# Performance work log

Hardware: AMD Instinct MI355X
Metric: run time of the kernel (lower is better)

## Reference

```python
import jax, jax.numpy as jnp
import numpy as np

B, S, E, D = 8, 2048, 512, 512  # batch, seq (mesh edges), elem_size, embd_size


def setup_inputs() -> dict:
    key = jax.random.key(0)
    ks = jax.random.split(key, 5)
    scale = 1.0 / np.sqrt(E)
    return {
        "x": jax.random.normal(ks[0], (B, S, E), dtype=jnp.float32),
        "Wq": jax.random.normal(ks[1], (E, D), dtype=jnp.float32) * scale,
        "bq": jax.random.normal(ks[2], (D,), dtype=jnp.float32) * 0.01,
        "Wk": jax.random.normal(ks[3], (E, D), dtype=jnp.float32) * scale,
        "bk": jax.random.normal(ks[4], (D,), dtype=jnp.float32) * 0.01,
    }


def reference(x, Wq, bq, Wk, bk):
    elem_size = x.shape[-1]
    q = jax.nn.relu(x @ Wq + bq)              # [B,S,D]
    k = jax.nn.relu(x @ Wk + bk)              # [B,S,D]
    scores = jnp.einsum("bqd,bkd->bqk", q, k) / (elem_size ** 0.5)  # [B,S,S]
    # nn.Softmax(dim=1): normalize over the QUERY axis (column-wise softmax)
    attn = jax.nn.softmax(scores, axis=1)
    new_values = jnp.einsum("bqk,bke->bqe", attn, x)  # V = raw x (use_V=False)
    return x + new_values                     # residual connection
```

## Files before the change

kernel.cpp:

```cpp
#include <hip/hip_runtime.h>
#include <hip/hip_bf16.h>
#include <math.h>

#define Bb 8
#define Ss 2048
#define Ee 512
#define Dd 512
#define QSPLIT 16

typedef __bf16 bf16x8 __attribute__((ext_vector_type(8)));
typedef __bf16 bf16x4 __attribute__((ext_vector_type(4)));
typedef float f32x4 __attribute__((ext_vector_type(4)));


__device__ __forceinline__ void stage64(ushort* lds, const __bf16* gbase,
                                        int ldg, int wave, int lane) {
#pragma unroll
    for (int t = 0; t < 4; ++t) {
        const int slot = wave * 256 + t * 64 + lane;
        const int row  = slot >> 3;
        const int c    = (slot & 7) ^ (row & 7);
        __builtin_amdgcn_global_load_lds(
            (const __attribute__((address_space(1))) void*)(gbase + (size_t)row * ldg + c * 8),
            (__attribute__((address_space(3))) void*)(lds + (size_t)slot * 8),
            16, 0, 0);
    }
}

__device__ __forceinline__ void stage64h(ushort* lds, const __bf16* gbase,
                                         int ldg, int wave, int lane) {
#pragma unroll
    for (int t = 0; t < 2; ++t) {
        const int slot = wave * 128 + t * 64 + lane;
        const int row  = slot >> 3;
        const int c    = (slot & 7) ^ (row & 7);
        __builtin_amdgcn_global_load_lds(
            (const __attribute__((address_space(1))) void*)(gbase + (size_t)row * ldg + c * 8),
            (__attribute__((address_space(3))) void*)(lds + (size_t)slot * 8),
            16, 0, 0);
    }
}

__device__ __forceinline__ void stage32(ushort* lds, const __bf16* gbase,
                                        int ldg, int wave, int lane) {
#pragma unroll
    for (int t = 0; t < 2; ++t) {
        const int slot = wave * 128 + t * 64 + lane;
        const int row  = slot >> 2;
        const int c    = (slot & 3) ^ ((row >> 1) & 3);
        __builtin_amdgcn_global_load_lds(
            (const __attribute__((address_space(1))) void*)(gbase + (size_t)row * ldg + c * 8),
            (__attribute__((address_space(3))) void*)(lds + (size_t)slot * 8),
            16, 0, 0);
    }
}

__global__ __launch_bounds__(256) void prep_fused(
    const float* __restrict__ x,
    const float* __restrict__ Wq, const float* __restrict__ Wk,
    __bf16* __restrict__ xb, __bf16* __restrict__ xT,
    __bf16* __restrict__ WqT, __bf16* __restrict__ WkT)
{
    __shared__ float tile[64][65];
    const int bid = blockIdx.x;
    const int tid = threadIdx.x;
    if (bid < 2048) {
        const int e0 = (bid & 7) * 64;
        const int s0 = ((bid >> 3) & 31) * 64;
        const int b  = bid >> 8;
        const float* ip = x + (size_t)b * Ss * Ee;
        __bf16* xbp = xb + (size_t)b * Ss * Ee;
        __bf16* xTp = xT + (size_t)b * Ee * Ss;
        const int rrow = tid >> 4;
        const int c4   = (tid & 15) * 4;
        #pragma unroll
        for (int it = 0; it < 4; ++it) {
            const int r = it * 16 + rrow;
            const float4 v = *(const float4*)&ip[(size_t)(s0 + r) * Ee + e0 + c4];
            bf16x4 h;
            h[0] = (__bf16)v.x; h[1] = (__bf16)v.y; h[2] = (__bf16)v.z; h[3] = (__bf16)v.w;
            *(bf16x4*)&xbp[(size_t)(s0 + r) * Ee + e0 + c4] = h;
            tile[r][c4 + 0] = v.x; tile[r][c4 + 1] = v.y;
            tile[r][c4 + 2] = v.z; tile[r][c4 + 3] = v.w;
        }
        __syncthreads();
        const int sc  = (tid & 7) * 8;
        const int erb = tid >> 3;
        #pragma unroll
        for (int it = 0; it < 2; ++it) {
            const int er = it * 32 + erb;
            bf16x8 o;
            #pragma unroll
            for (int t = 0; t < 8; ++t) o[t] = (__bf16)tile[sc + t][er];
            *(bf16x8*)&xTp[(size_t)(e0 + er) * Ss + s0 + sc] = o;
        }
    } else {
        const int t  = bid - 2048;
        const float* in = (t >> 8) ? Wk : Wq;
        __bf16* outp    = (t >> 8) ? WkT : WqT;
        const int x0 = (t & 15) * 32;
        const int y0 = ((t >> 4) & 15) * 32;
        const int tx = tid & 31, ty = tid >> 5;
        for (int i = ty; i < 32; i += 8)
            tile[i][tx] = in[(size_t)(y0 + i) * 512 + (x0 + tx)];
        __syncthreads();
        for (int i = ty; i < 32; i += 8)
            outp[(size_t)(x0 + i) * 512 + (y0 + tx)] = (__bf16)tile[tx][i];
    }
}

__global__ __launch_bounds__(256, 4) void proj_kernel(
    const __bf16* __restrict__ X,
    const __bf16* __restrict__ WqT, const __bf16* __restrict__ WkT,
    const float* __restrict__ bq, const float* __restrict__ bk,
    __bf16* __restrict__ qb, __bf16* __restrict__ kb)
{
    __shared__ __align__(16) ushort smem[4 * 128 * 32];
    ushort* As0 = smem;
    ushort* Bs0 = smem + 4096;
    ushort* As1 = smem + 8192;
    ushort* Bs1 = smem + 12288;
    const __bf16* WT  = blockIdx.z ? WkT : WqT;
    const float* bias = blockIdx.z ? bk : bq;
    __bf16* Out       = blockIdx.z ? kb : qb;

    const int tid = threadIdx.x;
    const int wave = tid >> 6, lane = tid & 63, quad = lane >> 4, l16 = lane & 15;
    const int wm = (wave >> 1) * 64, wn = (wave & 1) * 64;
    const int m0 = blockIdx.y * 128, n0 = blockIdx.x * 128;
    const int K = 512;
    const int swk = (quad ^ ((l16 >> 1) & 3)) * 8;

    f32x4 acc[4][4];
    f32x4 zero = {0.f, 0.f, 0.f, 0.f};
    for (int i = 0; i < 4; i++) for (int j = 0; j < 4; j++) acc[i][j] = zero;

    stage32(As0, X  + (size_t)m0 * K, K, wave, lane);
    stage32(Bs0, WT + (size_t)n0 * K, K, wave, lane);
    #pragma unroll 2
    for (int t = 0; t < 16; ++t) {
        ushort* Ac = (t & 1) ? As1 : As0;
        ushort* Bc = (t & 1) ? Bs1 : Bs0;
        if (t < 15) {
            ushort* An = (t & 1) ? As0 : As1;
            ushort* Bn = (t & 1) ? Bs0 : Bs1;
            const int kn = (t + 1) * 32;
            stage32(An, X  + (size_t)m0 * K + kn, K, wave, lane);
            stage32(Bn, WT + (size_t)n0 * K + kn, K, wave, lane);
            asm volatile("s_waitcnt vmcnt(4)" ::: "memory");
        } else {
            asm volatile("s_waitcnt vmcnt(0)" ::: "memory");
        }
        __builtin_amdgcn_s_barrier();
        bf16x8 af[4], bfr[4];
        for (int i = 0; i < 4; i++) af[i]  = *(bf16x8*)&Ac[(wm + i * 16 + l16) * 32 + swk];
        for (int j = 0; j < 4; j++) bfr[j] = *(bf16x8*)&Bc[(wn + j * 16 + l16) * 32 + swk];
        for (int i = 0; i < 4; i++)
            for (int j = 0; j < 4; j++)
                acc[i][j] = __builtin_amdgcn_mfma_f32_16x16x32_bf16(af[i], bfr[j], acc[i][j], 0, 0, 0);
        __builtin_amdgcn_sched_barrier(0);
        __builtin_amdgcn_s_barrier();
    }

    ushort* patch = smem + wave * 4096;
    for (int j = 0; j < 4; j++) {
        const float bv = bias[n0 + wn + j * 16 + l16];
        const int colsw = (j * 16 + l16) ^ (quad * 16);
        for (int i = 0; i < 4; i++)
            for (int rr = 0; rr < 4; rr++) {
                float v = acc[i][j][rr] + bv;
                v = v > 0.f ? v : 0.f;
                patch[(i * 16 + quad * 4 + rr) * 64 + colsw] = ((ushort2*)&v)[0].y;
            }
    }
    __syncthreads();
    #pragma unroll
    for (int it = 0; it < 8; it++) {
        const int lr = it * 8 + (lane >> 3);
        const int lc = ((lane & 7) * 8) ^ (((lr >> 2) & 3) * 16);
        const bf16x8 v = *(const bf16x8*)&patch[lr * 64 + lc];
        *(bf16x8*)&Out[(size_t)(m0 + wm + lr) * 512 + n0 + wn + (((lane & 7) * 8))] = v;
    }
}

__global__ __launch_bounds__(256, 4) void scores_kernel(
    const __bf16* __restrict__ Q,
    const __bf16* __restrict__ Km,
    __bf16* __restrict__ P,
    float* __restrict__ Lp)
{
    __shared__ __align__(16) ushort smem[4 * 128 * 32];
    __shared__ float stats[256];
    ushort* As0 = smem;
    ushort* Bs0 = smem + 4096;
    ushort* As1 = smem + 8192;
    ushort* Bs1 = smem + 12288;
    const int id = blockIdx.x;
    const int b = id & 7;
    const int rest = id >> 3;
    const int qy = rest >> 4;
    const int m0 = qy * 128;
    const int n0 = (rest & 15) * 128;
    const __bf16* A  = Q  + (size_t)b * Ss * Dd;
    const __bf16* Bp = Km + (size_t)b * Ss * Dd;
    __bf16* C = P + (size_t)b * Ss * Ss;

    const int tid = threadIdx.x;
    const int wave = tid >> 6, lane = tid & 63, quad = lane >> 4, l16 = lane & 15;
    const int wm = (wave >> 1) * 64, wn = (wave & 1) * 64;
    const int swk = (quad ^ ((l16 >> 1) & 3)) * 8;
    const float scale = 0.044194173824159216f;
    const float SHIFT = 8.0f;

    f32x4 acc[4][4];
    f32x4 zero = {0.f, 0.f, 0.f, 0.f};
    for (int i = 0; i < 4; i++) for (int j = 0; j < 4; j++) acc[i][j] = zero;

    stage32(As0, A  + (size_t)m0 * Dd, Dd, wave, lane);
    stage32(Bs0, Bp + (size_t)n0 * Dd, Dd, wave, lane);
    #pragma unroll 2
    for (int t = 0; t < 16; ++t) {
        ushort* Ac = (t & 1) ? As1 : As0;
        ushort* Bc = (t & 1) ? Bs1 : Bs0;
        if (t < 15) {
            ushort* An = (t & 1) ? As0 : As1;
            ushort* Bn = (t & 1) ? Bs0 : Bs1;
            const int kn = (t + 1) * 32;
            stage32(An, A  + (size_t)m0 * Dd + kn, Dd, wave, lane);
            stage32(Bn, Bp + (size_t)n0 * Dd + kn, Dd, wave, lane);
            asm volatile("s_waitcnt vmcnt(4)" ::: "memory");
        } else {
            asm volatile("s_waitcnt vmcnt(0)" ::: "memory");
        }
        __builtin_amdgcn_s_barrier();
        bf16x8 af[4], bfr[4];
        for (int i = 0; i < 4; i++) af[i]  = *(bf16x8*)&Ac[(wm + i * 16 + l16) * 32 + swk];
        for (int j = 0; j < 4; j++) bfr[j] = *(bf16x8*)&Bc[(wn + j * 16 + l16) * 32 + swk];
        for (int i = 0; i < 4; i++)
            for (int j = 0; j < 4; j++)
                acc[i][j] = __builtin_amdgcn_mfma_f32_16x16x32_bf16(af[i], bfr[j], acc[i][j], 0, 0, 0);
        __builtin_amdgcn_sched_barrier(0);
        __builtin_amdgcn_s_barrier();
    }

    float* Ls = stats;
    const int half = wave >> 1;
    ushort* patch = smem + wave * 4096;
    float lj[4];
    for (int j = 0; j < 4; j++) {
        float l = 0.f;
        const int colsw = (j * 16 + l16) ^ (quad * 16);
        for (int i = 0; i < 4; i++)
            for (int rr = 0; rr < 4; rr++) {
                const float e = __expf(fmaf(acc[i][j][rr], scale, -SHIFT));
                const __bf16 pb = (__bf16)e;
                patch[(i * 16 + quad * 4 + rr) * 64 + colsw] = *(const ushort*)&pb;
                l += e;
            }
        l += __shfl_xor(l, 16);
        l += __shfl_xor(l, 32);
        lj[j] = l;
    }
    if (quad == 0)
        for (int j = 0; j < 4; j++) Ls[half * 128 + wn + j * 16 + l16] = lj[j];
    __syncthreads();
    if (tid < 128) {
        const size_t o = ((size_t)qy * Bb + b) * Ss + n0 + tid;
        Lp[o] = Ls[tid] + Ls[128 + tid];
    }
    #pragma unroll
    for (int it = 0; it < 8; it++) {
        const int lr = it * 8 + (lane >> 3);
        const int lc = ((lane & 7) * 8) ^ (((lr >> 2) & 3) * 16);
        const bf16x8 v = *(const bf16x8*)&patch[lr * 64 + lc];
        *(bf16x8*)&C[(size_t)(m0 + wm + lr) * Ss + n0 + wn + ((lane & 7) * 8)] = v;
    }
}

__global__ __launch_bounds__(256) void csx_kernel(const float* __restrict__ Lp,
                                                  const __bf16* __restrict__ xT,
                                                  __bf16* __restrict__ XC) {
    __shared__ float cinv[2048];
    const int b = blockIdx.x >> 6;
    const int g = blockIdx.x & 63;
    const int tid = threadIdx.x;
    const int k0 = tid * 8;
    float s[8];
    #pragma unroll
    for (int u = 0; u < 8; ++u) s[u] = 0.f;
    for (int qy = 0; qy < QSPLIT; ++qy) {
        const float* lp = Lp + ((size_t)qy * Bb + b) * Ss + k0;
        const float4 a0 = *(const float4*)lp;
        const float4 a1 = *(const float4*)(lp + 4);
        s[0] += a0.x; s[1] += a0.y; s[2] += a0.z; s[3] += a0.w;
        s[4] += a1.x; s[5] += a1.y; s[6] += a1.z; s[7] += a1.w;
    }
    #pragma unroll
    for (int u = 0; u < 8; ++u) cinv[k0 + u] = 1.0f / s[u];
    __syncthreads();
    const float4 c0 = *(const float4*)&cinv[k0];
    const float4 c1 = *(const float4*)&cinv[k0 + 4];
    #pragma unroll
    for (int r = 0; r < 8; ++r) {
        const int e = g * 8 + r;
        const size_t base = ((size_t)b * Ee + e) * Ss;
        const bf16x8 v = *(const bf16x8*)&xT[base + k0];
        bf16x8 o;
        o[0] = (__bf16)((float)v[0] * c0.x);
        o[1] = (__bf16)((float)v[1] * c0.y);
        o[2] = (__bf16)((float)v[2] * c0.z);
        o[3] = (__bf16)((float)v[3] * c0.w);
        o[4] = (__bf16)((float)v[4] * c1.x);
        o[5] = (__bf16)((float)v[5] * c1.y);
        o[6] = (__bf16)((float)v[6] * c1.z);
        o[7] = (__bf16)((float)v[7] * c1.w);
        *(bf16x8*)&XC[base + k0] = o;
    }
}

__global__ __launch_bounds__(256, 4) void pv_kernel(
    const __bf16* __restrict__ P,
    const __bf16* __restrict__ XC,
    const __bf16* __restrict__ XB,
    float* __restrict__ Out)
{
    __shared__ __align__(16) ushort smem[2 * (64 * 64 + 128 * 64)];
    ushort* As0 = smem;
    ushort* Bs0 = smem + 4096;
    ushort* As1 = smem + 12288;
    ushort* Bs1 = smem + 16384;
    const int id = blockIdx.x;
    const int b = id & 7;
    const int rest = id >> 3;
    const int m0 = (rest >> 2) * 64;
    const int n0 = (rest & 3) * 128;
    const __bf16* A  = P  + (size_t)b * Ss * Ss;
    const __bf16* Bp = XC + (size_t)b * Ee * Ss;

    const int tid = threadIdx.x;
    const int wave = tid >> 6, lane = tid & 63, quad = lane >> 4, l16 = lane & 15;
    const int wm = (wave >> 1) * 32, wn = (wave & 1) * 64;
    const int sw0 = ((quad)     ^ (l16 & 7)) * 8;
    const int sw1 = ((quad + 4) ^ (l16 & 7)) * 8;

    f32x4 acc[2][4];
    f32x4 zero = {0.f, 0.f, 0.f, 0.f};
    for (int i = 0; i < 2; i++) for (int j = 0; j < 4; j++) acc[i][j] = zero;

    stage64h(As0, A  + (size_t)m0 * Ss, Ss, wave, lane);
    stage64 (Bs0, Bp + (size_t)n0 * Ss, Ss, wave, lane);
    #pragma unroll 2
    for (int t = 0; t < 32; ++t) {
        ushort* Ac = (t & 1) ? As1 : As0;
        ushort* Bc = (t & 1) ? Bs1 : Bs0;
        if (t < 31) {
            ushort* An = (t & 1) ? As0 : As1;
            ushort* Bn = (t & 1) ? Bs0 : Bs1;
            const int kn = (t + 1) * 64;
            stage64h(An, A  + (size_t)m0 * Ss + kn, Ss, wave, lane);
            stage64 (Bn, Bp + (size_t)n0 * Ss + kn, Ss, wave, lane);
            asm volatile("s_waitcnt vmcnt(6)" ::: "memory");
        } else {
            asm volatile("s_waitcnt vmcnt(0)" ::: "memory");
        }
        __builtin_amdgcn_s_barrier();
        #pragma unroll
        for (int h = 0; h < 2; h++) {
            const int sw = h ? sw1 : sw0;
            bf16x8 af[2], bfr[4];
            for (int i = 0; i < 2; i++) af[i]  = *(bf16x8*)&Ac[(wm + i * 16 + l16) * 64 + sw];
            for (int j = 0; j < 4; j++) bfr[j] = *(bf16x8*)&Bc[(wn + j * 16 + l16) * 64 + sw];
            for (int i = 0; i < 2; i++)
                for (int j = 0; j < 4; j++)
                    acc[i][j] = __builtin_amdgcn_mfma_f32_16x16x32_bf16(af[i], bfr[j], acc[i][j], 0, 0, 0);
        }
        __builtin_amdgcn_sched_barrier(0);
        __builtin_amdgcn_s_barrier();
    }

    for (int i = 0; i < 2; i++) {
        for (int j = 0; j < 4; j++) {
            const int col = n0 + wn + j * 16 + l16;
            for (int rr = 0; rr < 4; rr++) {
                const int row = m0 + wm + i * 16 + quad * 4 + rr;
                const size_t idx = ((size_t)b * Ss + row) * Ee + col;
                Out[idx] = (float)XB[idx] + acc[i][j][rr];
            }
        }
    }
}

extern "C" void kernel_launch(void* const* d_in, const int* in_sizes, int n_in,
                              void* d_out, int out_size, void* d_ws, size_t ws_size,
                              hipStream_t stream) {
    const float* x  = (const float*)d_in[0];
    const float* Wq = (const float*)d_in[1];
    const float* bq = (const float*)d_in[2];
    const float* Wk = (const float*)d_in[3];
    const float* bk = (const float*)d_in[4];
    float* out = (float*)d_out;

    char* ws = (char*)d_ws;
    size_t off = 0;
    auto alloc = [&](size_t bytes) -> void* {
        void* p = ws + off;
        off += (bytes + 255) & ~(size_t)255;
        return p;
    };
    __bf16* P    = (__bf16*)alloc((size_t)Bb * Ss * Ss * 2);
    __bf16* xb   = (__bf16*)alloc((size_t)Bb * Ss * Ee * 2);
    __bf16* qb   = (__bf16*)alloc((size_t)Bb * Ss * Dd * 2);
    __bf16* kb   = (__bf16*)alloc((size_t)Bb * Ss * Dd * 2);
    __bf16* xT   = (__bf16*)alloc((size_t)Bb * Ee * Ss * 2);
    __bf16* WqT  = (__bf16*)alloc((size_t)512 * 512 * 2);
    __bf16* WkT  = (__bf16*)alloc((size_t)512 * 512 * 2);
    float*  Lp   = (float*)alloc((size_t)QSPLIT * Bb * Ss * 4);
    if (off > ws_size) return;
    __bf16* XC = qb;

    prep_fused<<<dim3(2048 + 512), 256, 0, stream>>>(x, Wq, Wk, xb, xT, WqT, WkT);

    proj_kernel<<<dim3(4, 128, 2), 256, 0, stream>>>(xb, WqT, WkT, bq, bk, qb, kb);

    scores_kernel<<<dim3(2048), 256, 0, stream>>>(qb, kb, P, Lp);

    csx_kernel<<<dim3(512), 256, 0, stream>>>(Lp, xT, XC);

    pv_kernel<<<dim3(1024), 256, 0, stream>>>(P, XC, xb, out);
}
```

Measured before the change: 208.4 us.

## Drop LDS double buffering in scores and PV GEMMs for single-buffered K=64 loop

Replaces the double-buffered, software-pipelined K loops in the scores and PV kernels with a single LDS buffer. Each iteration now loads a tile, synchronizes, computes, and synchronizes again. In the scores kernel the K step also grows from 32 to 64, with the matching swizzle change, so there are fewer iterations. The aim is to shrink LDS use, which may allow more resident blocks and cuts barrier and waitcnt overhead. The cost is that global-to-LDS loads no longer overlap with the MFMA work.

```diff
diff --git a/kernel.cpp b/kernel.cpp
--- a/kernel.cpp
+++ b/kernel.cpp
@@ -189,12 +189,10 @@
     __bf16* __restrict__ P,
     float* __restrict__ Lp)
 {
-    __shared__ __align__(16) ushort smem[4 * 128 * 32];
+    __shared__ __align__(16) ushort smem[2 * 128 * 64];
     __shared__ float stats[256];
-    ushort* As0 = smem;
-    ushort* Bs0 = smem + 4096;
-    ushort* As1 = smem + 8192;
-    ushort* Bs1 = smem + 12288;
+    ushort* As = smem;
+    ushort* Bs = smem + 128 * 64;
     const int id = blockIdx.x;
     const int b = id & 7;
     const int rest = id >> 3;
@@ -208,7 +206,8 @@
     const int tid = threadIdx.x;
     const int wave = tid >> 6, lane = tid & 63, quad = lane >> 4, l16 = lane & 15;
     const int wm = (wave >> 1) * 64, wn = (wave & 1) * 64;
-    const int swk = (quad ^ ((l16 >> 1) & 3)) * 8;
+    const int sw0 = ((quad)     ^ (l16 & 7)) * 8;
+    const int sw1 = ((quad + 4) ^ (l16 & 7)) * 8;
     const float scale = 0.044194173824159216f;
     const float SHIFT = 8.0f;
 
@@ -216,31 +215,21 @@
     f32x4 zero = {0.f, 0.f, 0.f, 0.f};
     for (int i = 0; i < 4; i++) for (int j = 0; j < 4; j++) acc[i][j] = zero;
 
-    stage32(As0, A  + (size_t)m0 * Dd, Dd, wave, lane);
-    stage32(Bs0, Bp + (size_t)n0 * Dd, Dd, wave, lane);
-    #pragma unroll 2
-    for (int t = 0; t < 16; ++t) {
-        ushort* Ac = (t & 1) ? As1 : As0;
-        ushort* Bc = (t & 1) ? Bs1 : Bs0;
-        if (t < 15) {
-            ushort* An = (t & 1) ? As0 : As1;
-            ushort* Bn = (t & 1) ? Bs0 : Bs1;
-            const int kn = (t + 1) * 32;
-            stage32(An, A  + (size_t)m0 * Dd + kn, Dd, wave, lane);
-            stage32(Bn, Bp + (size_t)n0 * Dd + kn, Dd, wave, lane);
-            asm volatile("s_waitcnt vmcnt(4)" ::: "memory");
-        } else {
-            asm volatile("s_waitcnt vmcnt(0)" ::: "memory");
-        }
-        __builtin_amdgcn_s_barrier();
-        bf16x8 af[4], bfr[4];
-        for (int i = 0; i < 4; i++) af[i]  = *(bf16x8*)&Ac[(wm + i * 16 + l16) * 32 + swk];
-        for (int j = 0; j < 4; j++) bfr[j] = *(bf16x8*)&Bc[(wn + j * 16 + l16) * 32 + swk];
-        for (int i = 0; i < 4; i++)
-            for (int j = 0; j < 4; j++)
-                acc[i][j] = __builtin_amdgcn_mfma_f32_16x16x32_bf16(af[i], bfr[j], acc[i][j], 0, 0, 0);
-        __builtin_amdgcn_sched_barrier(0);
-        __builtin_amdgcn_s_barrier();
+    for (int k0 = 0; k0 < Dd; k0 += 64) {
+        stage64(As, A  + (size_t)m0 * Dd + k0, Dd, wave, lane);
+        stage64(Bs, Bp + (size_t)n0 * Dd + k0, Dd, wave, lane);
+        __syncthreads();
+        #pragma unroll
+        for (int h = 0; h < 2; h++) {
+            const int sw = h ? sw1 : sw0;
+            bf16x8 af[4], bfr[4];
+            for (int i = 0; i < 4; i++) af[i]  = *(bf16x8*)&As[(wm + i * 16 + l16) * 64 + sw];
+            for (int j = 0; j < 4; j++) bfr[j] = *(bf16x8*)&Bs[(wn + j * 16 + l16) * 64 + sw];
+            for (int i = 0; i < 4; i++)
+                for (int j = 0; j < 4; j++)
+                    acc[i][j] = __builtin_amdgcn_mfma_f32_16x16x32_bf16(af[i], bfr[j], acc[i][j], 0, 0, 0);
+        }
+        __syncthreads();
     }
 
     float* Ls = stats;
@@ -324,11 +313,9 @@
     const __bf16* __restrict__ XB,
     float* __restrict__ Out)
 {
-    __shared__ __align__(16) ushort smem[2 * (64 * 64 + 128 * 64)];
-    ushort* As0 = smem;
-    ushort* Bs0 = smem + 4096;
-    ushort* As1 = smem + 12288;
-    ushort* Bs1 = smem + 16384;
+    __shared__ __align__(16) ushort smem[64 * 64 + 128 * 64];
+    ushort* As = smem;
+    ushort* Bs = smem + 64 * 64;
     const int id = blockIdx.x;
     const int b = id & 7;
     const int rest = id >> 3;
@@ -347,35 +334,21 @@
     f32x4 zero = {0.f, 0.f, 0.f, 0.f};
     for (int i = 0; i < 2; i++) for (int j = 0; j < 4; j++) acc[i][j] = zero;
 
-    stage64h(As0, A  + (size_t)m0 * Ss, Ss, wave, lane);
-    stage64 (Bs0, Bp + (size_t)n0 * Ss, Ss, wave, lane);
-    #pragma unroll 2
-    for (int t = 0; t < 32; ++t) {
-        ushort* Ac = (t & 1) ? As1 : As0;
-        ushort* Bc = (t & 1) ? Bs1 : Bs0;
-        if (t < 31) {
-            ushort* An = (t & 1) ? As0 : As1;
-            ushort* Bn = (t & 1) ? Bs0 : Bs1;
-            const int kn = (t + 1) * 64;
-            stage64h(An, A  + (size_t)m0 * Ss + kn, Ss, wave, lane);
-            stage64 (Bn, Bp + (size_t)n0 * Ss + kn, Ss, wave, lane);
-            asm volatile("s_waitcnt vmcnt(6)" ::: "memory");
-        } else {
-            asm volatile("s_waitcnt vmcnt(0)" ::: "memory");
-        }
-        __builtin_amdgcn_s_barrier();
+    for (int k0 = 0; k0 < Ss; k0 += 64) {
+        stage64h(As, A  + (size_t)m0 * Ss + k0, Ss, wave, lane);
+        stage64 (Bs, Bp + (size_t)n0 * Ss + k0, Ss, wave, lane);
+        __syncthreads();
         #pragma unroll
         for (int h = 0; h < 2; h++) {
             const int sw = h ? sw1 : sw0;
             bf16x8 af[2], bfr[4];
-            for (int i = 0; i < 2; i++) af[i]  = *(bf16x8*)&Ac[(wm + i * 16 + l16) * 64 + sw];
-            for (int j = 0; j < 4; j++) bfr[j] = *(bf16x8*)&Bc[(wn + j * 16 + l16) * 64 + sw];
+            for (int i = 0; i < 2; i++) af[i]  = *(bf16x8*)&As[(wm + i * 16 + l16) * 64 + sw];
+            for (int j = 0; j < 4; j++) bfr[j] = *(bf16x8*)&Bs[(wn + j * 16 + l16) * 64 + sw];
             for (int i = 0; i < 2; i++)
                 for (int j = 0; j < 4; j++)
                     acc[i][j] = __builtin_amdgcn_mfma_f32_16x16x32_bf16(af[i], bfr[j], acc[i][j], 0, 0, 0);
         }
-        __builtin_amdgcn_sched_barrier(0);
-        __builtin_amdgcn_s_barrier();
+        __syncthreads();
     }
 
     for (int i = 0; i < 2; i++) {
```

Result: no change. 206.1 us (-1.1%).
